# Performance work log

Hardware: AMD Instinct MI355X
Metric: run time of the kernel (lower is better)

Reference implementation:

```python
import jax, jax.numpy as jnp
import numpy as np

N_NODES = 100000
N_EDGES = 1600000
D_IN, D_HID, D_OUT = 128, 128, 64


def _mean_agg(h_src_feat, src, dst, num_nodes):
    # gather source features along edges, scatter-sum into destinations,
    # divide by in-degree (clamped to 1, matching DGL zero-degree handling)
    summed = jax.ops.segment_sum(h_src_feat[src], dst, num_segments=num_nodes)
    deg = jax.ops.segment_sum(jnp.ones((src.shape[0],), h_src_feat.dtype), dst,
                              num_segments=num_nodes)
    return summed / jnp.maximum(deg, 1.0)[:, None]


def setup_inputs() -> dict:
    key = jax.random.key(0)
    ks = jax.random.split(key, 8)
    x = jax.random.normal(ks[0], (N_NODES, D_IN), dtype=jnp.float32)
    src = jax.random.randint(ks[1], (N_EDGES,), 0, N_NODES, dtype=jnp.int64)
    dst = jax.random.randint(ks[2], (N_EDGES,), 0, N_NODES, dtype=jnp.int64)
    s1 = 1.0 / np.sqrt(D_IN)
    s2 = 1.0 / np.sqrt(D_HID)
    W_self1 = jax.random.normal(ks[3], (D_IN, D_HID), dtype=jnp.float32) * s1
    W_neigh1 = jax.random.normal(ks[4], (D_IN, D_HID), dtype=jnp.float32) * s1
    b1 = jnp.zeros((D_HID,), dtype=jnp.float32)
    W_self2 = jax.random.normal(ks[5], (D_HID, D_OUT), dtype=jnp.float32) * s2
    W_neigh2 = jax.random.normal(ks[6], (D_HID, D_OUT), dtype=jnp.float32) * s2
    b2 = jnp.zeros((D_OUT,), dtype=jnp.float32)
    return {"x": x, "src": src, "dst": dst,
            "W_self1": W_self1, "W_neigh1": W_neigh1, "b1": b1,
            "W_self2": W_self2, "W_neigh2": W_neigh2, "b2": b2}


def reference(x, src, dst, W_self1, W_neigh1, b1, W_self2, W_neigh2, b2):
    n = x.shape[0]
    # layer 1: SAGEConv(mean) + ReLU (dropout is identity in eval mode)
    agg1 = _mean_agg(x, src, dst, n)
    h = x @ W_self1 + agg1 @ W_neigh1 + b1
    h = jax.nn.relu(h)
    # layer 2: SAGEConv(mean)
    agg2 = _mean_agg(h, src, dst, n)
    out = h @ W_self2 + agg2 @ W_neigh2 + b2
    return out
```

## Files before the change

kernel.cpp:

```cpp
#include <hip/hip_runtime.h>

#define N_NODES 100000
#define N_EDGES 1600000
#define D 128
#define D_OUT 64
#define MAXDEG 64

#define NBUCK 782
#define BSHIFT 7
#define BCAP  3072
#define NBLK_SPLIT 500
#define CHUNK 3200
#define NBLK_PACK 25

typedef __attribute__((ext_vector_type(8))) short short8;
typedef __attribute__((ext_vector_type(4))) float floatx4;
typedef __attribute__((ext_vector_type(2))) float floatx2;

__device__ inline unsigned short f2bf(float f) {
    unsigned u = __builtin_bit_cast(unsigned, f);
    u = (u + 0x7fffu + ((u >> 16) & 1u)) >> 16;
    return (unsigned short)u;
}
__device__ inline float bf2f(unsigned u16) {
    return __builtin_bit_cast(float, u16 << 16);
}

__device__ inline void pack_ncat(const float* __restrict__ Wa, const float* __restrict__ Wb,
                                 int ncA, int ncB, unsigned short* __restrict__ out, int t) {
    int nnt = (ncA + ncB) >> 4;
    int lane = t & 63;
    int nt = (t >> 6) % nnt;
    int kt = t / (64 * nnt);
    int col = nt * 16 + (lane & 15);
    int k0 = kt * 32 + ((lane >> 4) << 3);
    const float* W = (col < ncA) ? Wa : Wb;
    int nc = (col < ncA) ? ncA : ncB;
    int c  = (col < ncA) ? col : col - ncA;
    unsigned short* dstp = out + (size_t)((kt * nnt + nt) * 64 + lane) * 8;
    #pragma unroll
    for (int j = 0; j < 8; ++j)
        dstp[j] = f2bf(W[(size_t)(k0 + j) * nc + c]);
}

__global__ __launch_bounds__(256) void split_pack(
        const int* __restrict__ src, const int* __restrict__ dst,
        int* __restrict__ gcur, int* __restrict__ bucketbuf,
        const float* __restrict__ Ws1, const float* __restrict__ Wn1,
        const float* __restrict__ Ws2, const float* __restrict__ Wn2,
        unsigned short* __restrict__ Wp1, unsigned short* __restrict__ Wp2,
        unsigned char* __restrict__ y8, unsigned char* __restrict__ z8) {
    __shared__ int cnt[NBUCK];
    __shared__ int base_s[NBUCK];
    __shared__ int dstc[CHUNK];
    const int tid = threadIdx.x;
    const int b = blockIdx.x;
    if (b < NBLK_SPLIT) {
        const int e0 = b * CHUNK;
        for (int i = tid; i < NBUCK; i += 256) cnt[i] = 0;
        __syncthreads();
        for (int i = tid; i < CHUNK; i += 256) {
            int d = __builtin_nontemporal_load(dst + e0 + i);
            dstc[i] = d;
            atomicAdd(&cnt[d >> BSHIFT], 1);
        }
        __syncthreads();
        for (int i = tid; i < NBUCK; i += 256) {
            int c = cnt[i];
            base_s[i] = c ? atomicAdd(&gcur[i], c) : 0;
            cnt[i] = 0;
        }
        __syncthreads();
        for (int i = tid; i < CHUNK; i += 256) {
            int d = dstc[i];
            int s = __builtin_nontemporal_load(src + e0 + i);
            int bk = d >> BSHIFT;
            int p = base_s[bk] + atomicAdd(&cnt[bk], 1);
            if (p < BCAP)
                bucketbuf[bk * BCAP + p] = ((d & 127) << 17) | s;
        }
    } else {
        int sub = b - NBLK_SPLIT;
        if (sub < 16)      pack_ncat(Ws1, Wn1, D, D, Wp1, sub * 256 + tid);
        else if (sub < 24) pack_ncat(Ws2, Wn2, D_OUT, D_OUT, Wp2, (sub - 16) * 256 + tid);
        else {
            if (tid < 32)       ((unsigned*)(y8 + (size_t)N_NODES * 128))[tid] = 0;
            else if (tid < 48)  ((unsigned*)(z8 + (size_t)N_NODES * 64))[tid - 32] = 0;
        }
    }
}

__global__ __launch_bounds__(256) void csr_build(
        const int* __restrict__ gcur, const int* __restrict__ bucketbuf,
        int* __restrict__ dcount, int* __restrict__ csrp) {
    __shared__ int lcnt[128];
    const int tid = threadIdx.x, b = blockIdx.x;
    if (tid < 128) lcnt[tid] = 0;
    __syncthreads();
    int m = gcur[b]; if (m > BCAP) m = BCAP;
    const int* __restrict__ buf = bucketbuf + b * BCAP;
    for (int i = tid; i < m; i += 256) {
        int v = buf[i];
        int dloc = (v >> 17) & 127, s = v & 0x1FFFF;
        int node = (b << BSHIFT) + dloc;
        int slot = atomicAdd(&lcnt[dloc], 1);
        if (slot < MAXDEG && node < N_NODES)
            csrp[((size_t)node << 6) + slot] = s;
    }
    __syncthreads();
    if (tid < 128) {
        int node = (b << BSHIFT) + tid;
        if (node < N_NODES) {
            int c = lcnt[tid]; if (c > MAXDEG) c = MAXDEG;
            dcount[node] = c;
            int cf = (c + 15) & ~15; if (cf > MAXDEG) cf = MAXDEG;
            int* row = csrp + ((size_t)node << 6);
            for (int k = c; k < cf; ++k) row[k] = N_NODES;
        }
    }
}

template<int NTA, int NTB, bool AF32, bool OUTA_BF16>
__global__ __launch_bounds__(256) void gemm_dual(
        const void* __restrict__ A, const unsigned short* __restrict__ Wp,
        const float* __restrict__ bias, void* __restrict__ OutA,
        unsigned char* __restrict__ OutB)
{
    const int NT = NTA + NTB;
    const int wave = threadIdx.x >> 6;
    const int lane = threadIdx.x & 63;
    const int q = lane >> 4, m = lane & 15;

    int row = blockIdx.x * 64 + wave * 16 + m;
    int rowc = (row < N_NODES) ? row : (N_NODES - 1);

    floatx4 acc[NT];
    #pragma unroll
    for (int nt = 0; nt < NT; ++nt) acc[nt] = (floatx4){0.f, 0.f, 0.f, 0.f};

    #pragma unroll
    for (int kt = 0; kt < 4; ++kt) {
        short8 af;
        if (AF32) {
            const float* xr = (const float*)A + (size_t)rowc * D + kt * 32 + q * 8;
            float4 f0 = *(const float4*)xr;
            float4 f1 = *(const float4*)(xr + 4);
            af[0] = (short)f2bf(f0.x); af[1] = (short)f2bf(f0.y);
            af[2] = (short)f2bf(f0.z); af[3] = (short)f2bf(f0.w);
            af[4] = (short)f2bf(f1.x); af[5] = (short)f2bf(f1.y);
            af[6] = (short)f2bf(f1.z); af[7] = (short)f2bf(f1.w);
        } else {
            af = *(const short8*)((const unsigned short*)A +
                                  (size_t)rowc * D + kt * 32 + q * 8);
        }
        #pragma unroll
        for (int nt = 0; nt < NT; ++nt) {
            short8 bf = *(const short8*)(Wp + (size_t)((kt * NT + nt) * 64 + lane) * 8);
            acc[nt] = __builtin_amdgcn_mfma_f32_16x16x32_bf16(af, bf, acc[nt], 0, 0, 0);
        }
    }

    const int orow_base = blockIdx.x * 64 + wave * 16 + q * 4;
    #pragma unroll
    for (int nt = 0; nt < NT; ++nt) {
        float bv = (nt < NTA) ? bias[nt * 16 + m] : 0.f;
        #pragma unroll
        for (int i = 0; i < 4; ++i) {
            int orow = orow_base + i;
            if (orow < N_NODES) {
                float v = acc[nt][i];
                if (nt < NTA) {
                    v += bv;
                    if (OUTA_BF16)
                        ((unsigned short*)OutA)[(size_t)orow * (NTA * 16) + nt * 16 + m] = f2bf(v);
                    else
                        ((float*)OutA)[(size_t)orow * (NTA * 16) + nt * 16 + m] = v;
                } else {
                    int pk = __builtin_amdgcn_cvt_pk_fp8_f32(v, v, 0, false);
                    OutB[(size_t)orow * (NTB * 16) + (nt - NTA) * 16 + m] =
                        (unsigned char)(pk & 0xff);
                }
            }
        }
    }
}

template<bool L1>
__global__ __launch_bounds__(256) void agg_add(
        const unsigned char* __restrict__ feat, const int* __restrict__ csrp,
        const int* __restrict__ dcount, const void* __restrict__ self,
        void* __restrict__ out)
{
    const int LPE = L1 ? 32 : 16;
    const int EPG = 64 / LPE;
    const int FSH = L1 ? 7 : 6;
    const int NC  = L1 ? 128 : 64;

    int w = (blockIdx.x * 256 + threadIdx.x) >> 6;
    int lane = threadIdx.x & 63;
    if (w >= N_NODES) return;
    int dg = __builtin_amdgcn_readfirstlane(dcount[w]);
    const int g = lane / LPE;
    const int l = lane % LPE;
    int idxv = csrp[((size_t)w << 6) + lane];

    floatx2 ac0 = (floatx2){0.f, 0.f};
    floatx2 ac1 = (floatx2){0.f, 0.f};
    for (int j = 0; j < dg; j += 16) {
        #pragma unroll
        for (int u = 0; u < 16 / EPG; ++u) {
            int s = __shfl(idxv, j + u * EPG + g);
            unsigned v = *(const unsigned*)(feat + ((size_t)s << FSH) + (l << 2));
            ac0 += __builtin_amdgcn_cvt_pk_f32_fp8(v, false);
            ac1 += __builtin_amdgcn_cvt_pk_f32_fp8(v, true);
        }
    }
    #pragma unroll
    for (int delta = 32; delta >= LPE; delta >>= 1) {
        ac0.x += __shfl_down(ac0.x, delta); ac0.y += __shfl_down(ac0.y, delta);
        ac1.x += __shfl_down(ac1.x, delta); ac1.y += __shfl_down(ac1.y, delta);
    }
    if (g == 0) {
        float invd = (dg > 0) ? 1.0f / (float)dg : 1.0f;
        if (L1) {
            uint2 sv = *(const uint2*)((const unsigned short*)self + (size_t)w * NC + l * 4);
            float h0 = bf2f(sv.x & 0xffffu)  + ac0.x * invd;
            float h1 = bf2f(sv.x >> 16)      + ac0.y * invd;
            float h2 = bf2f(sv.y & 0xffffu)  + ac1.x * invd;
            float h3 = bf2f(sv.y >> 16)      + ac1.y * invd;
            h0 = fmaxf(h0, 0.f); h1 = fmaxf(h1, 0.f);
            h2 = fmaxf(h2, 0.f); h3 = fmaxf(h3, 0.f);
            uint2 pv;
            pv.x = (unsigned)f2bf(h0) | ((unsigned)f2bf(h1) << 16);
            pv.y = (unsigned)f2bf(h2) | ((unsigned)f2bf(h3) << 16);
            *(uint2*)((unsigned short*)out + (size_t)w * NC + l * 4) = pv;
        } else {
            const float* sp = (const float*)self + (size_t)w * NC + l * 4;
            float4 s0 = *(const float4*)sp;
            float4 o;
            o.x = s0.x + ac0.x * invd; o.y = s0.y + ac0.y * invd;
            o.z = s0.z + ac1.x * invd; o.w = s0.w + ac1.y * invd;
            *(float4*)((float*)out + (size_t)w * NC + l * 4) = o;
        }
    }
}

extern "C" void kernel_launch(void* const* d_in, const int* in_sizes, int n_in,
                              void* d_out, int out_size, void* d_ws, size_t ws_size,
                              hipStream_t stream) {
    const float* x   = (const float*)d_in[0];
    const int*   src = (const int*)d_in[1];
    const int*   dst = (const int*)d_in[2];
    const float* Ws1 = (const float*)d_in[3];
    const float* Wn1 = (const float*)d_in[4];
    const float* b1  = (const float*)d_in[5];
    const float* Ws2 = (const float*)d_in[6];
    const float* Wn2 = (const float*)d_in[7];
    const float* b2  = (const float*)d_in[8];
    float* out = (float*)d_out;

    const size_t nd = (size_t)N_NODES * D;
    unsigned short* h   = (unsigned short*)d_ws;
    unsigned short* xs  = h + nd;
    float*          tmp = (float*)xs;
    unsigned char*  y8  = (unsigned char*)(xs + nd);
    unsigned char*  z8  = y8 + (size_t)(N_NODES + 1) * D;
    int* dcount = (int*)(z8 + (size_t)(N_NODES + 1) * D_OUT);
    int* csrp   = dcount + N_NODES;
    int* gcur   = csrp + (size_t)N_NODES * MAXDEG;
    int* bucketbuf = gcur + 1024;
    unsigned short* Wp1 = (unsigned short*)(bucketbuf + (size_t)NBUCK * BCAP);
    unsigned short* Wp2 = Wp1 + 32768;

    hipMemsetAsync(gcur, 0, NBUCK * sizeof(int), stream);

    split_pack<<<NBLK_SPLIT + NBLK_PACK, 256, 0, stream>>>(
        src, dst, gcur, bucketbuf, Ws1, Wn1, Ws2, Wn2, Wp1, Wp2, y8, z8);
    csr_build<<<NBUCK, 256, 0, stream>>>(gcur, bucketbuf, dcount, csrp);

    const int gemm_blocks = (N_NODES + 63) / 64;
    const int agg_blocks  = (N_NODES * 64 + 255) / 256;

    gemm_dual<8, 8, true,  true ><<<gemm_blocks, 256, 0, stream>>>(x, Wp1, b1, xs, y8);
    agg_add<true ><<<agg_blocks, 256, 0, stream>>>(y8, csrp, dcount, xs, h);
    gemm_dual<4, 4, false, false><<<gemm_blocks, 256, 0, stream>>>(h, Wp2, b2, tmp, z8);
    agg_add<false><<<agg_blocks, 256, 0, stream>>>(z8, csrp, dcount, tmp, out);
}
```

Measured before the change: 298.9 us.

## Permute layer-1 feature layout so GEMM epilogue writes vectorized rows

The layer-1 dual GEMM now stores its bf16 self output and fp8 neighbour output in a column-interleaved order. Each lane then writes 16 contiguous bytes of bf16 and 8 contiguous bytes of fp8, replacing many scattered 2-byte and 1-byte stores. Because the aggregation works element by element, the hidden features stay in this permuted order, and the layer-2 weight packing permutes its K rows to match. The aim is to cut store transactions in the first GEMM, at the cost of a hidden coupling between the two layers' layout conventions.

```diff
diff --git a/kernel.cpp b/kernel.cpp
--- a/kernel.cpp
+++ b/kernel.cpp
@@ -26,6 +26,7 @@
     return __builtin_bit_cast(float, u16 << 16);
 }
 
+template<bool KPERM>
 __device__ inline void pack_ncat(const float* __restrict__ Wa, const float* __restrict__ Wb,
                                  int ncA, int ncB, unsigned short* __restrict__ out, int t) {
     int nnt = (ncA + ncB) >> 4;
@@ -39,8 +40,11 @@
     int c  = (col < ncA) ? col : col - ncA;
     unsigned short* dstp = out + (size_t)((kt * nnt + nt) * 64 + lane) * 8;
     #pragma unroll
-    for (int j = 0; j < 8; ++j)
-        dstp[j] = f2bf(W[(size_t)(k0 + j) * nc + c]);
+    for (int j = 0; j < 8; ++j) {
+        int k = k0 + j;
+        int kr = KPERM ? (((k & 7) << 4) | (k >> 3)) : k;
+        dstp[j] = f2bf(W[(size_t)kr * nc + c]);
+    }
 }
 
 __global__ __launch_bounds__(256) void split_pack(
@@ -81,8 +85,8 @@
         }
     } else {
         int sub = b - NBLK_SPLIT;
-        if (sub < 16)      pack_ncat(Ws1, Wn1, D, D, Wp1, sub * 256 + tid);
-        else if (sub < 24) pack_ncat(Ws2, Wn2, D_OUT, D_OUT, Wp2, (sub - 16) * 256 + tid);
+        if (sub < 16)      pack_ncat<false>(Ws1, Wn1, D, D, Wp1, sub * 256 + tid);
+        else if (sub < 24) pack_ncat<true >(Ws2, Wn2, D_OUT, D_OUT, Wp2, (sub - 16) * 256 + tid);
         else {
             if (tid < 32)       ((unsigned*)(y8 + (size_t)N_NODES * 128))[tid] = 0;
             else if (tid < 48)  ((unsigned*)(z8 + (size_t)N_NODES * 64))[tid - 32] = 0;
@@ -120,7 +124,7 @@
     }
 }
 
-template<int NTA, int NTB, bool AF32, bool OUTA_BF16>
+template<int NTA, int NTB, bool AF32, bool OUTA_BF16, bool ILV>
 __global__ __launch_bounds__(256) void gemm_dual(
         const void* __restrict__ A, const unsigned short* __restrict__ Wp,
         const float* __restrict__ bias, void* __restrict__ OutA,
@@ -161,24 +165,51 @@
     }
 
     const int orow_base = blockIdx.x * 64 + wave * 16 + q * 4;
-    #pragma unroll
-    for (int nt = 0; nt < NT; ++nt) {
-        float bv = (nt < NTA) ? bias[nt * 16 + m] : 0.f;
+    if (ILV) {
+        float bv[8];
+        #pragma unroll
+        for (int nt = 0; nt < 8; ++nt) bv[nt] = bias[nt * 16 + m];
         #pragma unroll
         for (int i = 0; i < 4; ++i) {
             int orow = orow_base + i;
             if (orow < N_NODES) {
-                float v = acc[nt][i];
-                if (nt < NTA) {
-                    v += bv;
-                    if (OUTA_BF16)
-                        ((unsigned short*)OutA)[(size_t)orow * (NTA * 16) + nt * 16 + m] = f2bf(v);
-                    else
-                        ((float*)OutA)[(size_t)orow * (NTA * 16) + nt * 16 + m] = v;
-                } else {
-                    int pk = __builtin_amdgcn_cvt_pk_fp8_f32(v, v, 0, false);
-                    OutB[(size_t)orow * (NTB * 16) + (nt - NTA) * 16 + m] =
-                        (unsigned char)(pk & 0xff);
+                unsigned w[4];
+                #pragma unroll
+                for (int t = 0; t < 4; ++t) {
+                    float v0 = acc[2 * t][i]     + bv[2 * t];
+                    float v1 = acc[2 * t + 1][i] + bv[2 * t + 1];
+                    w[t] = (unsigned)f2bf(v0) | ((unsigned)f2bf(v1) << 16);
+                }
+                uint4 pv; pv.x = w[0]; pv.y = w[1]; pv.z = w[2]; pv.w = w[3];
+                *(uint4*)((unsigned short*)OutA + (size_t)orow * 128 + m * 8) = pv;
+                int pk0 = __builtin_amdgcn_cvt_pk_fp8_f32(acc[8][i],  acc[9][i],  0,   false);
+                pk0     = __builtin_amdgcn_cvt_pk_fp8_f32(acc[10][i], acc[11][i], pk0, true);
+                int pk1 = __builtin_amdgcn_cvt_pk_fp8_f32(acc[12][i], acc[13][i], 0,   false);
+                pk1     = __builtin_amdgcn_cvt_pk_fp8_f32(acc[14][i], acc[15][i], pk1, true);
+                uint2 v8; v8.x = (unsigned)pk0; v8.y = (unsigned)pk1;
+                *(uint2*)(OutB + (size_t)orow * 128 + m * 8) = v8;
+            }
+        }
+    } else {
+        #pragma unroll
+        for (int nt = 0; nt < NT; ++nt) {
+            float bv = (nt < NTA) ? bias[nt * 16 + m] : 0.f;
+            #pragma unroll
+            for (int i = 0; i < 4; ++i) {
+                int orow = orow_base + i;
+                if (orow < N_NODES) {
+                    float v = acc[nt][i];
+                    if (nt < NTA) {
+                        v += bv;
+                        if (OUTA_BF16)
+                            ((unsigned short*)OutA)[(size_t)orow * (NTA * 16) + nt * 16 + m] = f2bf(v);
+                        else
+                            ((float*)OutA)[(size_t)orow * (NTA * 16) + nt * 16 + m] = v;
+                    } else {
+                        int pk = __builtin_amdgcn_cvt_pk_fp8_f32(v, v, 0, false);
+                        OutB[(size_t)orow * (NTB * 16) + (nt - NTA) * 16 + m] =
+                            (unsigned char)(pk & 0xff);
+                    }
                 }
             }
         }
@@ -281,8 +312,8 @@
     const int gemm_blocks = (N_NODES + 63) / 64;
     const int agg_blocks  = (N_NODES * 64 + 255) / 256;
 
-    gemm_dual<8, 8, true,  true ><<<gemm_blocks, 256, 0, stream>>>(x, Wp1, b1, xs, y8);
+    gemm_dual<8, 8, true,  true,  true ><<<gemm_blocks, 256, 0, stream>>>(x, Wp1, b1, xs, y8);
     agg_add<true ><<<agg_blocks, 256, 0, stream>>>(y8, csrp, dcount, xs, h);
-    gemm_dual<4, 4, false, false><<<gemm_blocks, 256, 0, stream>>>(h, Wp2, b2, tmp, z8);
+    gemm_dual<4, 4, false, false, false><<<gemm_blocks, 256, 0, stream>>>(h, Wp2, b2, tmp, z8);
     agg_add<false><<<agg_blocks, 256, 0, stream>>>(z8, csrp, dcount, tmp, out);
 }
```

Result: faster. 286.7 us (-4.1%).
